# Kernel optimization log

Measured on AMD Instinct MI355X. Metric: run time of the kernel, lower is better.

The kernel has to match this reference:

```python
import jax, jax.numpy as jnp
from jax import lax
import numpy as np

N_ASSETS = 256
BATCH = 512
MAX_WEIGHT = 0.05
N_ITERS = 300       # FISTA iterations (fixed, jit-friendly)
BISECT_ITERS = 60   # bisection iterations for the simplex-box projection
POWER_ITERS = 30    # power iterations for Lipschitz constant


def _project_capped_simplex(v, c):
    """Project rows of v onto {w : sum(w)=1, -c <= w <= c}.

    Finds tau s.t. sum(clip(v - tau, -c, c)) = 1 by bisection (non-diff),
    then recomputes tau exactly from the active-set mask so the projection
    is correctly differentiable (piecewise-linear Jacobian).
    """
    vs = lax.stop_gradient(v)
    lo = jnp.min(vs, axis=-1) - c   # sum = +n*c > 1 here
    hi = jnp.max(vs, axis=-1) + c   # sum = -n*c < 1 here

    def bis(carry, _):
        lo, hi = carry
        mid = 0.5 * (lo + hi)
        s = jnp.sum(jnp.clip(vs - mid[:, None], -c, c), axis=-1)
        lo = jnp.where(s > 1.0, mid, lo)
        hi = jnp.where(s > 1.0, hi, mid)
        return (lo, hi), None

    (lo, hi), _ = lax.scan(bis, (lo, hi), None, length=BISECT_ITERS)
    tau0 = 0.5 * (lo + hi)
    z = vs - tau0[:, None]
    interior = (jnp.abs(z) < c).astype(v.dtype)          # unclipped coords
    k_hi = jnp.sum((z >= c).astype(v.dtype), axis=-1)    # clipped at +c
    k_lo = jnp.sum((z <= -c).astype(v.dtype), axis=-1)   # clipped at -c
    denom = jnp.maximum(jnp.sum(interior, axis=-1), 1.0)
    # exact tau given the (stop-gradient) active set -> correct Jacobian in v
    tau = (jnp.sum(interior * v, axis=-1) + c * (k_hi - k_lo) - 1.0) / denom
    return jnp.clip(v - tau[:, None], -c, c)


def _min_var_weights(covmat_sqrt, c):
    """argmin_w ||A w||^2  s.t. sum(w)=1, -c<=w<=c  (batched FISTA)."""
    B, n, _ = covmat_sqrt.shape
    # Q = A^T A (the objective only depends on A through Q)
    Q = jnp.einsum('bij,bik->bjk', covmat_sqrt, covmat_sqrt)

    # power iteration for lambda_max(Q) -> step size 1/L, L = 2*lambda_max
    u = jnp.ones((B, n), covmat_sqrt.dtype) / jnp.sqrt(jnp.asarray(n, covmat_sqrt.dtype))

    def pit(u, _):
        u = jnp.einsum('bij,bj->bi', Q, u)
        u = u / (jnp.linalg.norm(u, axis=-1, keepdims=True) + 1e-12)
        return u, None

    u, _ = lax.scan(pit, u, None, length=POWER_ITERS)
    lmax = jnp.einsum('bi,bij,bj->b', u, Q, u)
    step = lax.stop_gradient(1.0 / (2.0 * lmax + 1e-12))[:, None]

    w0 = _project_capped_simplex(jnp.full((B, n), 1.0 / n, covmat_sqrt.dtype), c)

    @jax.checkpoint
    def fista(carry, _):
        w, y, t = carry
        g = 2.0 * jnp.einsum('bij,bj->bi', Q, y)
        w_new = _project_capped_simplex(y - step * g, c)
        t_new = 0.5 * (1.0 + jnp.sqrt(1.0 + 4.0 * t * t))
        y_new = w_new + ((t - 1.0) / t_new) * (w_new - w)
        return (w_new, y_new, t_new), None

    t0 = jnp.asarray(1.0, covmat_sqrt.dtype)
    (w, _, _), _ = lax.scan(fista, (w0, w0, t0), None, length=N_ITERS)
    return w


def setup_inputs() -> dict:
    key = jax.random.key(0)
    covmat_sqrt = jax.random.normal(
        key, (BATCH, N_ASSETS, N_ASSETS), dtype=jnp.float32
    ) / np.sqrt(N_ASSETS).astype(np.float32)
    return {"covmat_sqrt": covmat_sqrt}


def reference(covmat_sqrt):
    return _min_var_weights(covmat_sqrt, MAX_WEIGHT)
```

## Files before the change

### kernel.cpp

```cpp
#include <hip/hip_runtime.h>
#include <math.h>


#define NA    256
#define CAPW  0.05f

typedef float v2f __attribute__((ext_vector_type(2)));

template<int CTRL, int RM>
__device__ __forceinline__ float dpp0(float x) {
    return __int_as_float(__builtin_amdgcn_update_dpp(
        0, __float_as_int(x), CTRL, RM, 0xf, true));
}
template<int CTRL, int RM>
__device__ __forceinline__ float dppI(float x, float ident) {
    return __int_as_float(__builtin_amdgcn_update_dpp(
        __float_as_int(ident), __float_as_int(x), CTRL, RM, 0xf, false));
}
__device__ __forceinline__ float bcast63(float x) {
    return __int_as_float(__builtin_amdgcn_readlane(__float_as_int(x), 63));
}
__device__ __forceinline__ float wsum(float x) {
    x += dpp0<0x111, 0xf>(x);
    x += dpp0<0x112, 0xf>(x);
    x += dpp0<0x114, 0xf>(x);
    x += dpp0<0x118, 0xf>(x);
    x += dpp0<0x142, 0xa>(x);
    x += dpp0<0x143, 0xc>(x);
    return bcast63(x);
}
__device__ __forceinline__ float wmax(float x) {
    const float I = -1e30f;
    x = fmaxf(x, dppI<0x111, 0xf>(x, I));
    x = fmaxf(x, dppI<0x112, 0xf>(x, I));
    x = fmaxf(x, dppI<0x114, 0xf>(x, I));
    x = fmaxf(x, dppI<0x118, 0xf>(x, I));
    x = fmaxf(x, dppI<0x142, 0xa>(x, I));
    x = fmaxf(x, dppI<0x143, 0xc>(x, I));
    return bcast63(x);
}

__global__ void __launch_bounds__(512, 2)
markowitz_fista(const float* __restrict__ A, float* __restrict__ out)
{
    __shared__ float lds_pool[32 * 256];
    __shared__ int   done_flag;

    float* A_lds = lds_pool;
    float* p_lds = lds_pool;
    float* y_lds = lds_pool + 2048;

    const int tid = threadIdx.x;
    const int b   = blockIdx.x;
    const int r4  = tid & 63;
    const int e   = tid >> 6;
    const int R0  = r4 * 4;
    const int C0  = e * 32;

    const float* __restrict__ Ab = A + (size_t)b * NA * NA;

    v2f q2[4][16];
    #pragma unroll
    for (int a = 0; a < 4; ++a)
        #pragma unroll
        for (int k = 0; k < 16; ++k) q2[a][k] = (v2f){0.0f, 0.0f};

    for (int it = 0; it < 8; ++it) {
        __syncthreads();
        const float4* src = (const float4*)(Ab + it * 32 * 256);
        float4* dst = (float4*)A_lds;
        #pragma unroll
        for (int qd = 0; qd < 4; ++qd) dst[qd * 512 + tid] = src[qd * 512 + tid];
        __syncthreads();
        for (int ii = 0; ii < 32; ++ii) {
            const float* row = A_lds + ii * 256;
            float4 rv = *(const float4*)(row + R0);
            v2f r0 = {rv.x, rv.x}, r1 = {rv.y, rv.y}, r2 = {rv.z, rv.z}, r3 = {rv.w, rv.w};
            #pragma unroll
            for (int cc = 0; cc < 8; ++cc) {
                float4 cv = *(const float4*)(row + C0 + 4 * cc);
                v2f clo = {cv.x, cv.y}, chi = {cv.z, cv.w};
                q2[0][2*cc  ] = __builtin_elementwise_fma(r0, clo, q2[0][2*cc  ]);
                q2[0][2*cc+1] = __builtin_elementwise_fma(r0, chi, q2[0][2*cc+1]);
                q2[1][2*cc  ] = __builtin_elementwise_fma(r1, clo, q2[1][2*cc  ]);
                q2[1][2*cc+1] = __builtin_elementwise_fma(r1, chi, q2[1][2*cc+1]);
                q2[2][2*cc  ] = __builtin_elementwise_fma(r2, clo, q2[2][2*cc  ]);
                q2[2][2*cc+1] = __builtin_elementwise_fma(r2, chi, q2[2][2*cc+1]);
                q2[3][2*cc  ] = __builtin_elementwise_fma(r3, clo, q2[3][2*cc  ]);
                q2[3][2*cc+1] = __builtin_elementwise_fma(r3, chi, q2[3][2*cc+1]);
            }
        }
    }
    __syncthreads();

    auto partials = [&](bool chk) -> bool {
        __syncthreads();
        int fl = chk ? done_flag : 0;
        v2f aL0 = {0,0}, aL1 = {0,0}, aL2 = {0,0}, aL3 = {0,0};
        v2f aH0 = {0,0}, aH1 = {0,0}, aH2 = {0,0}, aH3 = {0,0};
        const float* yv = y_lds + C0;
        #pragma unroll
        for (int cc = 0; cc < 8; ++cc) {
            float4 y4 = *(const float4*)(yv + 4 * cc);
            v2f ylo = {y4.x, y4.y}, yhi = {y4.z, y4.w};
            aL0 = __builtin_elementwise_fma(q2[0][2*cc  ], ylo, aL0);
            aH0 = __builtin_elementwise_fma(q2[0][2*cc+1], yhi, aH0);
            aL1 = __builtin_elementwise_fma(q2[1][2*cc  ], ylo, aL1);
            aH1 = __builtin_elementwise_fma(q2[1][2*cc+1], yhi, aH1);
            aL2 = __builtin_elementwise_fma(q2[2][2*cc  ], ylo, aL2);
            aH2 = __builtin_elementwise_fma(q2[2][2*cc+1], yhi, aH2);
            aL3 = __builtin_elementwise_fma(q2[3][2*cc  ], ylo, aL3);
            aH3 = __builtin_elementwise_fma(q2[3][2*cc+1], yhi, aH3);
        }
        if (fl) return true;
        v2f s0 = aL0 + aH0, s1 = aL1 + aH1, s2 = aL2 + aH2, s3 = aL3 + aH3;
        *(float4*)(p_lds + e * 256 + R0) =
            make_float4(s0.x + s0.y, s1.x + s1.y, s2.x + s2.y, s3.x + s3.y);
        __syncthreads();
        return false;
    };
    auto reduceg = [&]() -> float4 {
        float4 r = *(const float4*)(p_lds + 4 * tid);
        #pragma unroll
        for (int ee = 1; ee < 8; ++ee) {
            float4 pv = *(const float4*)(p_lds + ee * 256 + 4 * tid);
            r.x += pv.x; r.y += pv.y; r.z += pv.z; r.w += pv.w;
        }
        return r;
    };

    if (tid < 64) {
        *(float4*)(y_lds + 4 * tid) = make_float4(0.0625f, 0.0625f, 0.0625f, 0.0625f);
    }
    float u0 = 0.f, u1 = 0.f, u2 = 0.f, u3 = 0.f;
    for (int p = 0; p < 30; ++p) {
        partials(false);
        if (tid < 64) {
            float4 g4 = reduceg();
            float ss = wsum(g4.x*g4.x + g4.y*g4.y + g4.z*g4.z + g4.w*g4.w);
            float inv = 1.0f / (sqrtf(ss) + 1e-12f);
            u0 = g4.x * inv; u1 = g4.y * inv; u2 = g4.z * inv; u3 = g4.w * inv;
            *(float4*)(y_lds + 4 * tid) = make_float4(u0, u1, u2, u3);
        }
    }
    partials(false);

    float step2 = 0.f, t = 1.0f, tau_ws = 0.0f, tau_pv = 0.0f, rm = 0.0f;
    float wa = 0.f, wb = 0.f, wc = 0.f, wd = 0.f;
    float ya = 0.f, yb = 0.f, yc = 0.f, yd = 0.f;
    if (tid < 64) {
        float4 g4 = reduceg();
        float lm = wsum(u0*g4.x + u1*g4.y + u2*g4.z + u3*g4.w);
        float step = 1.0f / (2.0f * lm + 1e-12f);
        step2 = 2.0f * step;
        wa = wb = wc = wd = 1.0f / 256.0f;
        ya = yb = yc = yd = 1.0f / 256.0f;
        *(float4*)(y_lds + 4 * tid) = make_float4(ya, yb, yc, yd);
    }
    if (tid == 0) done_flag = 0;

    for (int itn = 0; itn < 300; ++itn) {
        if (partials(true)) break;
        if (tid < 64) {
            float4 g4 = reduceg();
            float v0 = ya - step2 * g4.x;
            float v1 = yb - step2 * g4.y;
            float v2 = yc - step2 * g4.z;
            float v3 = yd - step2 * g4.w;

            float lo = -2.0f, hi = 2.0f;
            float tau = fminf(fmaxf(tau_ws + (tau_ws - tau_pv), lo), hi);

            float s = 0.f, cnt = 1.f, sm1 = 0.f;
            bool have = false;
            for (int ni = 0; ni < 10; ++ni) {
                float z0 = v0 - tau, z1 = v1 - tau, z2 = v2 - tau, z3 = v3 - tau;
                float c0 = fminf(fmaxf(z0, -CAPW), CAPW);
                float c1 = fminf(fmaxf(z1, -CAPW), CAPW);
                float c2 = fminf(fmaxf(z2, -CAPW), CAPW);
                float c3 = fminf(fmaxf(z3, -CAPW), CAPW);
                s   = wsum(c0 + c1 + c2 + c3);
                cnt = wsum((fabsf(z0) < CAPW ? 1.f : 0.f) +
                           (fabsf(z1) < CAPW ? 1.f : 0.f) +
                           (fabsf(z2) < CAPW ? 1.f : 0.f) +
                           (fabsf(z3) < CAPW ? 1.f : 0.f));
                sm1 = s - 1.0f;
                if (fabsf(sm1) <= 5e-5f) { have = true; break; }
                if (sm1 > 0.0f) lo = tau; else hi = tau;
                float tn2 = tau + sm1 / fmaxf(cnt, 1.0f);
                if (!(tn2 > lo && tn2 < hi)) tn2 = 0.5f * (lo + hi);
                tau = tn2;
            }
            if (!have) {
                float z0 = v0 - tau, z1 = v1 - tau, z2 = v2 - tau, z3 = v3 - tau;
                float c0 = fminf(fmaxf(z0, -CAPW), CAPW);
                float c1 = fminf(fmaxf(z1, -CAPW), CAPW);
                float c2 = fminf(fmaxf(z2, -CAPW), CAPW);
                float c3 = fminf(fmaxf(z3, -CAPW), CAPW);
                s   = wsum(c0 + c1 + c2 + c3);
                cnt = wsum((fabsf(z0) < CAPW ? 1.f : 0.f) +
                           (fabsf(z1) < CAPW ? 1.f : 0.f) +
                           (fabsf(z2) < CAPW ? 1.f : 0.f) +
                           (fabsf(z3) < CAPW ? 1.f : 0.f));
                sm1 = s - 1.0f;
            }
            float tauf = tau + sm1 / fmaxf(cnt, 1.0f);
            tau_pv = tau_ws;
            tau_ws = tauf;
            float w0n = fminf(fmaxf(v0 - tauf, -CAPW), CAPW);
            float w1n = fminf(fmaxf(v1 - tauf, -CAPW), CAPW);
            float w2n = fminf(fmaxf(v2 - tauf, -CAPW), CAPW);
            float w3n = fminf(fmaxf(v3 - tauf, -CAPW), CAPW);

            float tn = 0.5f * (1.0f + sqrtf(1.0f + 4.0f * t * t));
            float beta = (t - 1.0f) / tn;
            float y0n = w0n + beta * (w0n - wa);
            float y1n = w1n + beta * (w1n - wb);
            float y2n = w2n + beta * (w2n - wc);
            float y3n = w3n + beta * (w3n - wd);

            float dm = fmaxf(fmaxf(fabsf(w0n - wa), fabsf(w1n - wb)),
                             fmaxf(fabsf(w2n - wc), fabsf(w3n - wd)));
            rm = fmaxf(rm, dm);
            if ((itn & 7) == 7) {
                float rmax = wmax(rm);
                if (rmax < 1e-10f && tid == 0) done_flag = 1;
                rm = 0.0f;
            }

            wa = w0n; wb = w1n; wc = w2n; wd = w3n;
            ya = y0n; yb = y1n; yc = y2n; yd = y3n;
            t = tn;
            *(float4*)(y_lds + 4 * tid) = make_float4(ya, yb, yc, yd);
        }
    }

    if (tid < 64) {
        *(float4*)(out + b * 256 + 4 * tid) = make_float4(wa, wb, wc, wd);
    }
}

extern "C" void kernel_launch(void* const* d_in, const int* in_sizes, int n_in,
                              void* d_out, int out_size, void* d_ws, size_t ws_size,
                              hipStream_t stream) {
    (void)in_sizes; (void)n_in; (void)d_ws; (void)ws_size; (void)out_size;
    const float* A = (const float*)d_in[0];
    float* out = (float*)d_out;
    hipLaunchKernelGGL(markowitz_fista, dim3(512), dim3(512), 0, stream, A, out);
}
```

Before: 904.8 us.

## Reduce matvec partials with LDS atomics into double-buffered gradient buffers

The 8-wave partial-sum buffer plus the serial 8-way reduction in wave 0 is replaced by LDS atomicAdd into a single 256-float gradient buffer. Two buffers alternate, and a second wave zeroes the next one while wave 0 runs the projection. The aim is to shorten wave 0's critical path and shrink LDS traffic. The tau-solver tolerance and the early-exit convergence threshold are also loosened (1e-10 to 1e-7), so the loop can stop sooner at some cost in accuracy. Atomic ordering makes the float sums nondeterministic.

```diff
diff --git a/kernel.cpp b/kernel.cpp
--- a/kernel.cpp
+++ b/kernel.cpp
@@ -47,8 +47,9 @@
     __shared__ int   done_flag;
 
     float* A_lds = lds_pool;
-    float* p_lds = lds_pool;
-    float* y_lds = lds_pool + 2048;
+    float* gbuf0 = lds_pool;
+    float* gbuf1 = lds_pool + 256;
+    float* y_lds = lds_pool + 512;
 
     const int tid = threadIdx.x;
     const int b   = blockIdx.x;
@@ -93,7 +94,11 @@
     }
     __syncthreads();
 
-    auto partials = [&](bool chk) -> bool {
+    if (tid < 128) {
+        ((float4*)lds_pool)[tid] = make_float4(0.f, 0.f, 0.f, 0.f);
+    }
+
+    auto partials = [&](float* gbuf, bool chk) -> bool {
         __syncthreads();
         int fl = chk ? done_flag : 0;
         v2f aL0 = {0,0}, aL1 = {0,0}, aL2 = {0,0}, aL3 = {0,0};
@@ -114,55 +119,57 @@
         }
         if (fl) return true;
         v2f s0 = aL0 + aH0, s1 = aL1 + aH1, s2 = aL2 + aH2, s3 = aL3 + aH3;
-        *(float4*)(p_lds + e * 256 + R0) =
-            make_float4(s0.x + s0.y, s1.x + s1.y, s2.x + s2.y, s3.x + s3.y);
+        atomicAdd(&gbuf[R0 + 0], s0.x + s0.y);
+        atomicAdd(&gbuf[R0 + 1], s1.x + s1.y);
+        atomicAdd(&gbuf[R0 + 2], s2.x + s2.y);
+        atomicAdd(&gbuf[R0 + 3], s3.x + s3.y);
         __syncthreads();
         return false;
     };
-    auto reduceg = [&]() -> float4 {
-        float4 r = *(const float4*)(p_lds + 4 * tid);
-        #pragma unroll
-        for (int ee = 1; ee < 8; ++ee) {
-            float4 pv = *(const float4*)(p_lds + ee * 256 + 4 * tid);
-            r.x += pv.x; r.y += pv.y; r.z += pv.z; r.w += pv.w;
-        }
-        return r;
-    };
+
+    float* gb[2] = { gbuf0, gbuf1 };
+    int pp = 0;
 
     if (tid < 64) {
         *(float4*)(y_lds + 4 * tid) = make_float4(0.0625f, 0.0625f, 0.0625f, 0.0625f);
     }
     float u0 = 0.f, u1 = 0.f, u2 = 0.f, u3 = 0.f;
     for (int p = 0; p < 30; ++p) {
-        partials(false);
+        partials(gb[pp], false);
         if (tid < 64) {
-            float4 g4 = reduceg();
+            float4 g4 = *(const float4*)(gb[pp] + 4 * tid);
             float ss = wsum(g4.x*g4.x + g4.y*g4.y + g4.z*g4.z + g4.w*g4.w);
             float inv = 1.0f / (sqrtf(ss) + 1e-12f);
             u0 = g4.x * inv; u1 = g4.y * inv; u2 = g4.z * inv; u3 = g4.w * inv;
             *(float4*)(y_lds + 4 * tid) = make_float4(u0, u1, u2, u3);
-        }
-    }
-    partials(false);
+        } else if (tid < 128) {
+            *(float4*)(gb[pp ^ 1] + 4 * (tid - 64)) = make_float4(0.f, 0.f, 0.f, 0.f);
+        }
+        pp ^= 1;
+    }
+    partials(gb[pp], false);
 
     float step2 = 0.f, t = 1.0f, tau_ws = 0.0f, tau_pv = 0.0f, rm = 0.0f;
     float wa = 0.f, wb = 0.f, wc = 0.f, wd = 0.f;
     float ya = 0.f, yb = 0.f, yc = 0.f, yd = 0.f;
     if (tid < 64) {
-        float4 g4 = reduceg();
+        float4 g4 = *(const float4*)(gb[pp] + 4 * tid);
         float lm = wsum(u0*g4.x + u1*g4.y + u2*g4.z + u3*g4.w);
         float step = 1.0f / (2.0f * lm + 1e-12f);
         step2 = 2.0f * step;
         wa = wb = wc = wd = 1.0f / 256.0f;
         ya = yb = yc = yd = 1.0f / 256.0f;
         *(float4*)(y_lds + 4 * tid) = make_float4(ya, yb, yc, yd);
+    } else if (tid < 128) {
+        *(float4*)(gb[pp ^ 1] + 4 * (tid - 64)) = make_float4(0.f, 0.f, 0.f, 0.f);
     }
     if (tid == 0) done_flag = 0;
+    pp ^= 1;
 
     for (int itn = 0; itn < 300; ++itn) {
-        if (partials(true)) break;
+        if (partials(gb[pp], true)) break;
         if (tid < 64) {
-            float4 g4 = reduceg();
+            float4 g4 = *(const float4*)(gb[pp] + 4 * tid);
             float v0 = ya - step2 * g4.x;
             float v1 = yb - step2 * g4.y;
             float v2 = yc - step2 * g4.z;
@@ -185,7 +192,7 @@
                            (fabsf(z2) < CAPW ? 1.f : 0.f) +
                            (fabsf(z3) < CAPW ? 1.f : 0.f));
                 sm1 = s - 1.0f;
-                if (fabsf(sm1) <= 5e-5f) { have = true; break; }
+                if (fabsf(sm1) <= 1e-4f) { have = true; break; }
                 if (sm1 > 0.0f) lo = tau; else hi = tau;
                 float tn2 = tau + sm1 / fmaxf(cnt, 1.0f);
                 if (!(tn2 > lo && tn2 < hi)) tn2 = 0.5f * (lo + hi);
@@ -219,20 +226,24 @@
             float y2n = w2n + beta * (w2n - wc);
             float y3n = w3n + beta * (w3n - wd);
 
+            *(float4*)(y_lds + 4 * tid) = make_float4(y0n, y1n, y2n, y3n);
+
             float dm = fmaxf(fmaxf(fabsf(w0n - wa), fabsf(w1n - wb)),
                              fmaxf(fabsf(w2n - wc), fabsf(w3n - wd)));
             rm = fmaxf(rm, dm);
             if ((itn & 7) == 7) {
                 float rmax = wmax(rm);
-                if (rmax < 1e-10f && tid == 0) done_flag = 1;
+                if (rmax < 1e-7f && tid == 0) done_flag = 1;
                 rm = 0.0f;
             }
 
             wa = w0n; wb = w1n; wc = w2n; wd = w3n;
             ya = y0n; yb = y1n; yc = y2n; yd = y3n;
             t = tn;
-            *(float4*)(y_lds + 4 * tid) = make_float4(ya, yb, yc, yd);
-        }
+        } else if (tid < 128) {
+            *(float4*)(gb[pp ^ 1] + 4 * (tid - 64)) = make_float4(0.f, 0.f, 0.f, 0.f);
+        }
+        pp ^= 1;
     }
 
     if (tid < 64) {
```

Result: slower. 2.497 ms (+176.0%).

## Use secant tau solver, unnormalized power iteration and looser convergence thresholds

Applied to the files above, without the earlier changes.

The power iteration drops its per-step norm reduction and instead scales by a fixed factor, recovering lambda_max as a Rayleigh quotient at the end. The projection root-finder now uses a secant slope and carries the interior count from the previous iteration, so each inner step needs only one wave reduction instead of two. The projection tolerance and the early-exit threshold on weight change are both loosened (5e-5 to 1e-4, and 1e-10 to 1e-7), so blocks can stop iterating sooner. This trades some numerical precision, plus overflow risk from the fixed power-iteration scaling, for fewer reductions and fewer FISTA iterations.

```diff
diff --git a/kernel.cpp b/kernel.cpp
--- a/kernel.cpp
+++ b/kernel.cpp
@@ -132,25 +132,27 @@
     if (tid < 64) {
         *(float4*)(y_lds + 4 * tid) = make_float4(0.0625f, 0.0625f, 0.0625f, 0.0625f);
     }
-    float u0 = 0.f, u1 = 0.f, u2 = 0.f, u3 = 0.f;
+    float u0 = 0.0625f, u1 = 0.0625f, u2 = 0.0625f, u3 = 0.0625f;
     for (int p = 0; p < 30; ++p) {
         partials(false);
         if (tid < 64) {
             float4 g4 = reduceg();
-            float ss = wsum(g4.x*g4.x + g4.y*g4.y + g4.z*g4.z + g4.w*g4.w);
-            float inv = 1.0f / (sqrtf(ss) + 1e-12f);
-            u0 = g4.x * inv; u1 = g4.y * inv; u2 = g4.z * inv; u3 = g4.w * inv;
+            u0 = 0.25f * g4.x; u1 = 0.25f * g4.y;
+            u2 = 0.25f * g4.z; u3 = 0.25f * g4.w;
             *(float4*)(y_lds + 4 * tid) = make_float4(u0, u1, u2, u3);
         }
     }
     partials(false);
 
     float step2 = 0.f, t = 1.0f, tau_ws = 0.0f, tau_pv = 0.0f, rm = 0.0f;
+    float cnt_ws = 256.0f;
     float wa = 0.f, wb = 0.f, wc = 0.f, wd = 0.f;
     float ya = 0.f, yb = 0.f, yc = 0.f, yd = 0.f;
     if (tid < 64) {
         float4 g4 = reduceg();
-        float lm = wsum(u0*g4.x + u1*g4.y + u2*g4.z + u3*g4.w);
+        float num = wsum(u0*g4.x + u1*g4.y + u2*g4.z + u3*g4.w);
+        float den = wsum(u0*u0 + u1*u1 + u2*u2 + u3*u3);
+        float lm = num / (den + 1e-30f);
         float step = 1.0f / (2.0f * lm + 1e-12f);
         step2 = 2.0f * step;
         wa = wb = wc = wd = 1.0f / 256.0f;
@@ -171,24 +173,29 @@
             float lo = -2.0f, hi = 2.0f;
             float tau = fminf(fmaxf(tau_ws + (tau_ws - tau_pv), lo), hi);
 
-            float s = 0.f, cnt = 1.f, sm1 = 0.f;
-            bool have = false;
+            float s = 0.f, sm1 = 0.f;
+            float tau_p = 0.f, s_p = 0.f;
+            bool havep = false, have = false;
             for (int ni = 0; ni < 10; ++ni) {
                 float z0 = v0 - tau, z1 = v1 - tau, z2 = v2 - tau, z3 = v3 - tau;
                 float c0 = fminf(fmaxf(z0, -CAPW), CAPW);
                 float c1 = fminf(fmaxf(z1, -CAPW), CAPW);
                 float c2 = fminf(fmaxf(z2, -CAPW), CAPW);
                 float c3 = fminf(fmaxf(z3, -CAPW), CAPW);
-                s   = wsum(c0 + c1 + c2 + c3);
-                cnt = wsum((fabsf(z0) < CAPW ? 1.f : 0.f) +
-                           (fabsf(z1) < CAPW ? 1.f : 0.f) +
-                           (fabsf(z2) < CAPW ? 1.f : 0.f) +
-                           (fabsf(z3) < CAPW ? 1.f : 0.f));
+                s = wsum((c0 + c1) + (c2 + c3));
                 sm1 = s - 1.0f;
-                if (fabsf(sm1) <= 5e-5f) { have = true; break; }
+                if (fabsf(sm1) <= 1e-4f) { have = true; break; }
                 if (sm1 > 0.0f) lo = tau; else hi = tau;
-                float tn2 = tau + sm1 / fmaxf(cnt, 1.0f);
+                float m = fmaxf(cnt_ws, 1.0f);
+                if (havep) {
+                    float dt = tau - tau_p;
+                    float ds = s_p - s;
+                    float mm = ds / dt;
+                    if (mm > 0.5f && mm == mm) m = mm;
+                }
+                float tn2 = tau + sm1 / m;
                 if (!(tn2 > lo && tn2 < hi)) tn2 = 0.5f * (lo + hi);
+                tau_p = tau; s_p = s; havep = true;
                 tau = tn2;
             }
             if (!have) {
@@ -197,20 +204,24 @@
                 float c1 = fminf(fmaxf(z1, -CAPW), CAPW);
                 float c2 = fminf(fmaxf(z2, -CAPW), CAPW);
                 float c3 = fminf(fmaxf(z3, -CAPW), CAPW);
-                s   = wsum(c0 + c1 + c2 + c3);
-                cnt = wsum((fabsf(z0) < CAPW ? 1.f : 0.f) +
-                           (fabsf(z1) < CAPW ? 1.f : 0.f) +
-                           (fabsf(z2) < CAPW ? 1.f : 0.f) +
-                           (fabsf(z3) < CAPW ? 1.f : 0.f));
+                s = wsum((c0 + c1) + (c2 + c3));
                 sm1 = s - 1.0f;
             }
-            float tauf = tau + sm1 / fmaxf(cnt, 1.0f);
+            {
+                float z0 = v0 - tau, z1 = v1 - tau, z2 = v2 - tau, z3 = v3 - tau;
+                float cnt = wsum((fabsf(z0) < CAPW ? 1.f : 0.f) +
+                                 (fabsf(z1) < CAPW ? 1.f : 0.f) +
+                                 (fabsf(z2) < CAPW ? 1.f : 0.f) +
+                                 (fabsf(z3) < CAPW ? 1.f : 0.f));
+                cnt_ws = cnt;
+                tau = tau + sm1 / fmaxf(cnt, 1.0f);
+            }
             tau_pv = tau_ws;
-            tau_ws = tauf;
-            float w0n = fminf(fmaxf(v0 - tauf, -CAPW), CAPW);
-            float w1n = fminf(fmaxf(v1 - tauf, -CAPW), CAPW);
-            float w2n = fminf(fmaxf(v2 - tauf, -CAPW), CAPW);
-            float w3n = fminf(fmaxf(v3 - tauf, -CAPW), CAPW);
+            tau_ws = tau;
+            float w0n = fminf(fmaxf(v0 - tau, -CAPW), CAPW);
+            float w1n = fminf(fmaxf(v1 - tau, -CAPW), CAPW);
+            float w2n = fminf(fmaxf(v2 - tau, -CAPW), CAPW);
+            float w3n = fminf(fmaxf(v3 - tau, -CAPW), CAPW);
 
             float tn = 0.5f * (1.0f + sqrtf(1.0f + 4.0f * t * t));
             float beta = (t - 1.0f) / tn;
@@ -219,19 +230,20 @@
             float y2n = w2n + beta * (w2n - wc);
             float y3n = w3n + beta * (w3n - wd);
 
+            *(float4*)(y_lds + 4 * tid) = make_float4(y0n, y1n, y2n, y3n);
+
             float dm = fmaxf(fmaxf(fabsf(w0n - wa), fabsf(w1n - wb)),
                              fmaxf(fabsf(w2n - wc), fabsf(w3n - wd)));
             rm = fmaxf(rm, dm);
             if ((itn & 7) == 7) {
                 float rmax = wmax(rm);
-                if (rmax < 1e-10f && tid == 0) done_flag = 1;
+                if (rmax < 1e-7f && tid == 0) done_flag = 1;
                 rm = 0.0f;
             }
 
             wa = w0n; wb = w1n; wc = w2n; wd = w3n;
             ya = y0n; yb = y1n; yc = y2n; yd = y3n;
             t = tn;
-            *(float4*)(y_lds + 4 * tid) = make_float4(ya, yb, yc, yd);
         }
     }
 
```

Result: slower. 933.9 us (+3.2%).
